# Kernel optimization log

Hardware: AMD Instinct MI355X
Metric: run time of the kernel (lower is better)

The kernel has to match this reference:

```python
import jax, jax.numpy as jnp
import numpy as np

V, E, H, K, B, T = 50000, 128, 256, 9, 128, 512
HD = H // 2  # hidden per direction


def setup_inputs() -> dict:
    key = jax.random.key(0)
    ks = jax.random.split(key, 16)
    s = 0.1
    inp = {
        "x": jax.random.randint(ks[0], (B, T), 0, V),
        "emb": jax.random.normal(ks[1], (V, E), jnp.float32) * 0.02,
        "w_ih_f": jax.random.normal(ks[2], (4 * HD, E), jnp.float32) * s,
        "w_hh_f": jax.random.normal(ks[3], (4 * HD, HD), jnp.float32) * s,
        "b_ih_f": jax.random.normal(ks[4], (4 * HD,), jnp.float32) * s,
        "b_hh_f": jax.random.normal(ks[5], (4 * HD,), jnp.float32) * s,
        "w_ih_b": jax.random.normal(ks[6], (4 * HD, E), jnp.float32) * s,
        "w_hh_b": jax.random.normal(ks[7], (4 * HD, HD), jnp.float32) * s,
        "b_ih_b": jax.random.normal(ks[8], (4 * HD,), jnp.float32) * s,
        "b_hh_b": jax.random.normal(ks[9], (4 * HD,), jnp.float32) * s,
        "W_tag": jax.random.normal(ks[10], (K, H), jnp.float32) * s,
        "b_tag": jax.random.normal(ks[11], (K,), jnp.float32) * s,
        "start_trans": jax.random.normal(ks[12], (K,), jnp.float32) * s,
        "end_trans": jax.random.normal(ks[13], (K,), jnp.float32) * s,
        "trans": jax.random.normal(ks[14], (K, K), jnp.float32) * s,
    }
    return inp


def _lstm_dir(xs, w_ih, w_hh, b_ih, b_hh, reverse):
    # xs: [T, B, E]; PyTorch gate order: i, f, g, o
    Bsz = xs.shape[1]
    hd = w_hh.shape[1]
    b = b_ih + b_hh

    def step(carry, x_t):
        h, c = carry
        gates = x_t @ w_ih.T + h @ w_hh.T + b  # [B, 4*hd]
        i, f, g, o = jnp.split(gates, 4, axis=-1)
        i = jax.nn.sigmoid(i)
        f = jax.nn.sigmoid(f)
        g = jnp.tanh(g)
        o = jax.nn.sigmoid(o)
        c = f * c + i * g
        h = o * jnp.tanh(c)
        return (h, c), h

    init = (jnp.zeros((Bsz, hd), xs.dtype), jnp.zeros((Bsz, hd), xs.dtype))
    _, hs = jax.lax.scan(step, init, xs, reverse=reverse)
    return hs  # [T, B, hd], time-ordered


def _viterbi(emissions, start_trans, end_trans, trans):
    # emissions: [T, B, K]; returns best tag path [B, T] (torchcrf decode, no mask)
    score0 = start_trans[None, :] + emissions[0]  # [B, K]

    def step(score, emis_t):
        # score[b, i] + trans[i, j] -> best over i
        cand = score[:, :, None] + trans[None, :, :]  # [B, K, K]
        bp = jnp.argmax(cand, axis=1)                 # [B, K] best prev tag
        best = jnp.max(cand, axis=1)
        return best + emis_t, bp

    final_score, bps = jax.lax.scan(step, score0, emissions[1:])  # bps: [T-1, B, K]
    final_score = final_score + end_trans[None, :]
    last_tag = jnp.argmax(final_score, axis=-1)  # [B]

    def back(tag, bp):
        prev = jnp.take_along_axis(bp, tag[:, None], axis=1)[:, 0]
        return prev, prev

    _, path = jax.lax.scan(back, last_tag, bps, reverse=True)  # [T-1, B]
    tags = jnp.concatenate([path, last_tag[None, :]], axis=0)  # [T, B]
    return tags.T.astype(jnp.int32)  # [B, T]


def reference(x, emb, w_ih_f, w_hh_f, b_ih_f, b_hh_f,
              w_ih_b, w_hh_b, b_ih_b, b_hh_b,
              W_tag, b_tag, start_trans, end_trans, trans):
    xt = x.T                        # [T, B]
    e = emb[xt]                     # [T, B, E] embedding gather
    h_f = _lstm_dir(e, w_ih_f, w_hh_f, b_ih_f, b_hh_f, reverse=False)
    h_b = _lstm_dir(e, w_ih_b, w_hh_b, b_ih_b, b_hh_b, reverse=True)
    h = jnp.concatenate([h_f, h_b], axis=-1)  # [T, B, H]
    # dropout is identity at inference
    emissions = h @ W_tag.T + b_tag           # [T, B, K]
    return _viterbi(emissions, start_trans, end_trans, trans)
```

## Files before the change

kernel.cpp:

```cpp
#include <hip/hip_runtime.h>
#include <math.h>

#define TT 512
#define BB 128
#define KK 9

__device__ __forceinline__ float fast_sigmoid(float x) {
    const float LOG2E = 1.4426950408889634f;
    float e = __builtin_amdgcn_exp2f(-x * LOG2E);
    return __builtin_amdgcn_rcpf(1.0f + e);
}
__device__ __forceinline__ float fast_tanh(float x) {
    const float LOG2E = 1.4426950408889634f;
    float a = fabsf(x);
    float e = __builtin_amdgcn_exp2f(-2.0f * a * LOG2E);
    float t = (1.0f - e) * __builtin_amdgcn_rcpf(1.0f + e);
    return copysignf(t, x);
}

__global__ __launch_bounds__(256, 3) void input_gemm(
    const int* __restrict__ x, const float* __restrict__ emb,
    const float* __restrict__ w_ih_f, const float* __restrict__ w_ih_b,
    const float* __restrict__ b_ih_f, const float* __restrict__ b_hh_f,
    const float* __restrict__ b_ih_b, const float* __restrict__ b_hh_b,
    float* __restrict__ buf_f, float* __restrict__ buf_b,
    int t0f, int t0b)
{
    const int dir = blockIdx.z;
    const int s   = blockIdx.x;
    const int n0  = blockIdx.y * 128;
    const int t   = (dir ? t0b : t0f) + s;
    const float* w  = dir ? w_ih_b : w_ih_f;
    const float* bi = dir ? b_ih_b : b_ih_f;
    const float* bh = dir ? b_hh_b : b_hh_f;
    float* dst = dir ? buf_b : buf_f;

    __shared__ __align__(16) float As[32][132];
    __shared__ __align__(16) float Bs[32][132];

    const int tid  = threadIdx.x;
    const int lrow = tid >> 3;
    const int k4   = (tid & 7) * 4;

    int tokr[4];
    #pragma unroll
    for (int p = 0; p < 4; p++) tokr[p] = x[(p * 32 + lrow) * TT + t];

    const int tx = tid & 15;
    const int ty = tid >> 4;

    float acc[8][8];
    #pragma unroll
    for (int i = 0; i < 8; i++)
        #pragma unroll
        for (int j = 0; j < 8; j++) acc[i][j] = 0.0f;

    float4 aS[4], bS[4];
    #pragma unroll
    for (int p = 0; p < 4; p++) {
        aS[p] = *(const float4*)(emb + (size_t)tokr[p] * 128 + k4);
        bS[p] = *(const float4*)(w + (size_t)(n0 + p * 32 + lrow) * 128 + k4);
    }

    for (int kc = 0; kc < 128; kc += 32) {
        __syncthreads();
        #pragma unroll
        for (int p = 0; p < 4; p++) {
            const int row = p * 32 + lrow;
            As[k4 + 0][row] = aS[p].x; As[k4 + 1][row] = aS[p].y;
            As[k4 + 2][row] = aS[p].z; As[k4 + 3][row] = aS[p].w;
            Bs[k4 + 0][row] = bS[p].x; Bs[k4 + 1][row] = bS[p].y;
            Bs[k4 + 2][row] = bS[p].z; Bs[k4 + 3][row] = bS[p].w;
        }
        __syncthreads();
        if (kc + 32 < 128) {
            #pragma unroll
            for (int p = 0; p < 4; p++) {
                aS[p] = *(const float4*)(emb + (size_t)tokr[p] * 128 + kc + 32 + k4);
                bS[p] = *(const float4*)(w + (size_t)(n0 + p * 32 + lrow) * 128 + kc + 32 + k4);
            }
        }
        #pragma unroll 8
        for (int k = 0; k < 32; k++) {
            float4 af0 = *(const float4*)&As[k][ty * 8];
            float4 af1 = *(const float4*)&As[k][ty * 8 + 4];
            float4 bf0 = *(const float4*)&Bs[k][tx * 4];
            float4 bf1 = *(const float4*)&Bs[k][64 + tx * 4];
            float a_[8] = {af0.x, af0.y, af0.z, af0.w, af1.x, af1.y, af1.z, af1.w};
            float b_[8] = {bf0.x, bf0.y, bf0.z, bf0.w, bf1.x, bf1.y, bf1.z, bf1.w};
            #pragma unroll
            for (int i = 0; i < 8; i++)
                #pragma unroll
                for (int j = 0; j < 8; j++)
                    acc[i][j] += a_[i] * b_[j];
        }
    }

    const int nb0 = n0 + tx * 4;
    const int nb1 = n0 + 64 + tx * 4;
    float bias[8];
    #pragma unroll
    for (int j = 0; j < 4; j++) {
        bias[j]     = bi[nb0 + j] + bh[nb0 + j];
        bias[4 + j] = bi[nb1 + j] + bh[nb1 + j];
    }
    #pragma unroll
    for (int i = 0; i < 8; i++) {
        int brow = ty * 8 + i;
        float* o = dst + ((size_t)s * 128 + brow) * 512;
        float4 v0, v1;
        v0.x = acc[i][0] + bias[0]; v0.y = acc[i][1] + bias[1];
        v0.z = acc[i][2] + bias[2]; v0.w = acc[i][3] + bias[3];
        v1.x = acc[i][4] + bias[4]; v1.y = acc[i][5] + bias[5];
        v1.z = acc[i][6] + bias[6]; v1.w = acc[i][7] + bias[7];
        *(float4*)(o + nb0) = v0;
        *(float4*)(o + nb1) = v1;
    }
}

__global__ __launch_bounds__(512, 2) void lstm_fused(
    const float* __restrict__ buf_f, const float* __restrict__ buf_b,
    const float* __restrict__ w_hh_f, const float* __restrict__ w_hh_b,
    float* __restrict__ h_all,
    float* __restrict__ h_state, float* __restrict__ c_state,
    const float* __restrict__ W_tag, const float* __restrict__ b_tag,
    const float* __restrict__ start_trans, const float* __restrict__ end_trans,
    const float* __restrict__ trans,
    float* __restrict__ emB, unsigned* __restrict__ flags,
    int* __restrict__ out,
    int t0f, int t0b, int C, int init, int tail)
{
    const int dir = blockIdx.x >> 7;
    const int b   = blockIdx.x & 127;
    const int j   = threadIdx.x;
    const int w_  = j >> 6;
    const int l   = j & 63;
    const int m   = l >> 2;
    const int q   = l & 3;
    const int k   = w_ * 16 + m;
    const int r   = q * 128 + k;

    unsigned snap = 0u;
    if (tail && dir == 0 && j == 0)
        snap = __hip_atomic_load(&flags[b], __ATOMIC_RELAXED, __HIP_MEMORY_SCOPE_AGENT);

    const float* whh = dir ? w_hh_b : w_hh_f;
    float wR[128];
    #pragma unroll
    for (int qq = 0; qq < 32; qq++) {
        float4 v = *(const float4*)(whh + (size_t)r * 128 + qq * 4);
        wR[4*qq+0] = v.x; wR[4*qq+1] = v.y; wR[4*qq+2] = v.z; wR[4*qq+3] = v.w;
    }

    __shared__ __align__(16) float h_lds[2][128];
    __shared__ __align__(16) float wt_s[KK * 132];
    __shared__ __align__(16) float em_s[TT * KK];
    __shared__ __align__(16) float h_tile[64 * 132];
    __shared__ unsigned char bp[TT][KK];
    __shared__ int bj_s;

    float c;
    if (init) {
        c = 0.0f;
        if (q == 0) h_lds[0][k] = 0.0f;
    } else {
        c = c_state[((size_t)dir * 128 + b) * 128 + k];
        if (q == 0) h_lds[0][k] = h_state[((size_t)dir * 128 + b) * 128 + k];
    }
    __syncthreads();

    const float* buf = dir ? buf_b : buf_f;
    const int t0     = dir ? t0b : t0f;
    const int  tl0   = dir ? (C - 1) : 0;
    const long lstep = dir ? -(long)(128 * 512) : (long)(128 * 512);

    const float* xp = buf + ((size_t)tl0 * 128 + b) * 512 + r;
    float xw = *xp;
    float h_reg = 0.0f;

    float* hdst = h_all + (size_t)(dir * BB + b) * TT * 128;

    for (int s = 0; s < C; s++) {
        const int t = t0 + (dir ? (C - 1 - s) : s);
        const int p = s & 1;
        const float* hprev = h_lds[p];

        float a0 = 0.f, a1 = 0.f, a2 = 0.f, a3 = 0.f;
        #pragma unroll
        for (int qq = 0; qq < 32; qq++) {
            float4 h4 = *(const float4*)&hprev[4 * qq];
            a0 += wR[4*qq+0] * h4.x;
            a1 += wR[4*qq+1] * h4.y;
            a2 += wR[4*qq+2] * h4.z;
            a3 += wR[4*qq+3] * h4.w;
        }
        float pre = xw + ((a0 + a1) + (a2 + a3));

        float act = (q == 2) ? fast_tanh(pre) : fast_sigmoid(pre);

        float f_ = __shfl_xor(act, 1);
        float g_ = __shfl_xor(act, 2);
        float o_ = __shfl_xor(act, 3);

        c = f_ * c + act * g_;
        h_reg = o_ * fast_tanh(c);
        if (q == 0) h_lds[p ^ 1][k] = h_reg;

        __syncthreads();

        if (s + 1 < C) { xp += lstep; xw = *xp; }
        if (q == 0)
            hdst[(size_t)t * 128 + k] = h_reg;
    }

    if (q == 0) {
        h_state[((size_t)dir * 128 + b) * 128 + k] = h_reg;
        c_state[((size_t)dir * 128 + b) * 128 + k] = c;
    }

    if (!tail) return;

    for (int f = j; f < KK * 128; f += 512)
        wt_s[(f >> 7) * 132 + (f & 127)] = W_tag[(f >> 7) * 256 + dir * 128 + (f & 127)];

    float* emdst = emB + (size_t)b * TT * KK;

    for (int tile = 0; tile < TT / 64; tile++) {
        const int tb = tile * 64;
        __syncthreads();
        #pragma unroll
        for (int it = 0; it < 4; it++) {
            const int f4 = it * 512 + j;
            const int tr = f4 >> 5;
            const int c4 = (f4 & 31) * 4;
            float4 v = *(const float4*)(hdst + (size_t)(tb + tr) * 128 + c4);
            *(float4*)&h_tile[tr * 132 + c4] = v;
        }
        __syncthreads();
        for (int task = j; task < 64 * KK; task += 512) {
            const int tl = task / 9;
            const int kk = task - tl * 9;
            const float* hp = &h_tile[tl * 132];
            const float* wp = &wt_s[kk * 132];
            float acc = 0.0f;
            #pragma unroll
            for (int i4 = 0; i4 < 32; i4++) {
                float4 h4 = *(const float4*)(hp + i4 * 4);
                float4 w4 = *(const float4*)(wp + i4 * 4);
                acc += h4.x * w4.x + h4.y * w4.y + h4.z * w4.z + h4.w * w4.w;
            }
            if (dir == 1) emdst[(size_t)tb * KK + task] = acc;
            else          em_s[tb * KK + task] = acc;
        }
    }
    __syncthreads();

    if (dir == 1) {
        if (j == 0) {
            __threadfence();
            __hip_atomic_fetch_add(&flags[b], 1u, __ATOMIC_RELEASE,
                                   __HIP_MEMORY_SCOPE_AGENT);
        }
        return;
    }

    if (j == 0) {
        while (__hip_atomic_load(&flags[b], __ATOMIC_ACQUIRE,
                                 __HIP_MEMORY_SCOPE_AGENT) == snap)
            __builtin_amdgcn_s_sleep(1);
    }
    __syncthreads();
    for (int f = j; f < TT * KK; f += 512)
        em_s[f] += emdst[f] + b_tag[f % KK];
    __syncthreads();

    if (j < 64) {
        const int lane = j;

        float trans_col[KK];
        float score = -1e30f;
        if (lane < KK) {
            #pragma unroll
            for (int i = 0; i < KK; i++) trans_col[i] = trans[i * KK + lane];
            score = start_trans[lane] + em_s[lane];
        }

        float em_cur = (lane < KK) ? em_s[KK + lane] : 0.0f;
        for (int t = 1; t < TT; t++) {
            float em_next = (t + 1 < TT && lane < KK) ? em_s[(t + 1) * KK + lane] : 0.0f;

            float my = (lane < KK) ? score : -1e30f;
            float cand[KK];
            #pragma unroll
            for (int i = 0; i < KK; i++) cand[i] = __shfl(my, i) + trans_col[i];

            float v01, v23, v45, v67, v03, v47, v07, vb_;
            int   i01, i23, i45, i67, i03, i47, i07, ib_;
            {
                bool gt;
                gt = cand[1] > cand[0]; v01 = gt ? cand[1] : cand[0]; i01 = gt ? 1 : 0;
                gt = cand[3] > cand[2]; v23 = gt ? cand[3] : cand[2]; i23 = gt ? 3 : 2;
                gt = cand[5] > cand[4]; v45 = gt ? cand[5] : cand[4]; i45 = gt ? 5 : 4;
                gt = cand[7] > cand[6]; v67 = gt ? cand[7] : cand[6]; i67 = gt ? 7 : 6;
                gt = v23 > v01; v03 = gt ? v23 : v01; i03 = gt ? i23 : i01;
                gt = v67 > v45; v47 = gt ? v67 : v45; i47 = gt ? i67 : i45;
                gt = v47 > v03; v07 = gt ? v47 : v03; i07 = gt ? i47 : i03;
                gt = cand[8] > v07; vb_ = gt ? cand[8] : v07; ib_ = gt ? 8 : i07;
            }

            if (lane < KK) {
                bp[t][lane] = (unsigned char)ib_;
                score = vb_ + em_cur;
            }
            em_cur = em_next;
        }

        float fin = (lane < KK) ? (score + end_trans[lane]) : -1e30f;
        float farr[KK];
        #pragma unroll
        for (int jx = 0; jx < KK; jx++) farr[jx] = __shfl(fin, jx);
        float v01, v23, v45, v67, v03, v47, v07, vb_;
        int   i01, i23, i45, i67, i03, i47, i07, bj;
        {
            bool gt;
            gt = farr[1] > farr[0]; v01 = gt ? farr[1] : farr[0]; i01 = gt ? 1 : 0;
            gt = farr[3] > farr[2]; v23 = gt ? farr[3] : farr[2]; i23 = gt ? 3 : 2;
            gt = farr[5] > farr[4]; v45 = gt ? farr[5] : farr[4]; i45 = gt ? 5 : 4;
            gt = farr[7] > farr[6]; v67 = gt ? farr[7] : farr[6]; i67 = gt ? 7 : 6;
            gt = v23 > v01; v03 = gt ? v23 : v01; i03 = gt ? i23 : i01;
            gt = v67 > v45; v47 = gt ? v67 : v45; i47 = gt ? i67 : i45;
            gt = v47 > v03; v07 = gt ? v47 : v03; i07 = gt ? i47 : i03;
            gt = farr[8] > v07; vb_ = gt ? farr[8] : v07; bj = gt ? 8 : i07;
        }

        if (lane == 0) {
            bj_s = bj;
            out[b * TT + (TT - 1)] = bj;
        }
    }
    __syncthreads();

    {
        unsigned char* mA = (unsigned char*)h_tile;
        unsigned char* mB = mA + TT * KK;
        #pragma unroll
        for (int i = 0; i < KK; i++)
            mA[j * KK + i] = (j >= 1) ? bp[j][i] : (unsigned char)0;
        __syncthreads();
        for (int kk = 1; kk < TT; kk <<= 1) {
            if (j >= 1) {
                if (j + kk < TT) {
                    #pragma unroll
                    for (int i = 0; i < KK; i++)
                        mB[j * KK + i] = mA[j * KK + mA[(j + kk) * KK + i]];
                } else {
                    #pragma unroll
                    for (int i = 0; i < KK; i++)
                        mB[j * KK + i] = mA[j * KK + i];
                }
            }
            __syncthreads();
            unsigned char* tmp = mA; mA = mB; mB = tmp;
        }
        if (j >= 1)
            out[b * TT + (j - 1)] = mA[j * KK + bj_s];
    }
}

extern "C" void kernel_launch(void* const* d_in, const int* in_sizes, int n_in,
                              void* d_out, int out_size, void* d_ws, size_t ws_size,
                              hipStream_t stream)
{
    const int*   x       = (const int*)  d_in[0];
    const float* emb     = (const float*)d_in[1];
    const float* w_ih_f  = (const float*)d_in[2];
    const float* w_hh_f  = (const float*)d_in[3];
    const float* b_ih_f  = (const float*)d_in[4];
    const float* b_hh_f  = (const float*)d_in[5];
    const float* w_ih_b  = (const float*)d_in[6];
    const float* w_hh_b  = (const float*)d_in[7];
    const float* b_ih_b  = (const float*)d_in[8];
    const float* b_hh_b  = (const float*)d_in[9];
    const float* W_tag   = (const float*)d_in[10];
    const float* b_tag   = (const float*)d_in[11];
    const float* start_t = (const float*)d_in[12];
    const float* end_t   = (const float*)d_in[13];
    const float* trans   = (const float*)d_in[14];
    int* out = (int*)d_out;

    const size_t em_elems    = (size_t)BB * TT * KK;
    const size_t state_elems = (size_t)2 * 128 * 128;
    const size_t hall_elems  = (size_t)2 * BB * TT * 128;

    int C = 32;
    const int cands[5] = {512, 256, 128, 64, 32};
    for (int ci = 0; ci < 5; ci++) {
        size_t need = ((size_t)2 * cands[ci] * BB * 512
                       + em_elems + 2 * state_elems + hall_elems) * sizeof(float)
                      + 1024;
        if (ws_size >= need) { C = cands[ci]; break; }
    }

    float* buf_f   = (float*)d_ws;
    float* buf_b   = buf_f + (size_t)C * BB * 512;
    float* emB     = buf_b + (size_t)C * BB * 512;
    float* h_state = emB + em_elems;
    float* c_state = h_state + state_elems;
    float* h_all   = c_state + state_elems;
    unsigned* flags = (unsigned*)(h_all + hall_elems);

    const int rounds = TT / C;
    for (int r = 0; r < rounds; r++) {
        const int t0f = r * C;
        const int t0b = TT - (r + 1) * C;
        dim3 gg(C, 4, 2);
        input_gemm<<<gg, dim3(256), 0, stream>>>(
            x, emb, w_ih_f, w_ih_b, b_ih_f, b_hh_f, b_ih_b, b_hh_b,
            buf_f, buf_b, t0f, t0b);
        lstm_fused<<<dim3(256), dim3(512), 0, stream>>>(
            buf_f, buf_b, w_hh_f, w_hh_b, h_all,
            h_state, c_state,
            W_tag, b_tag, start_t, end_t, trans,
            emB, flags, out,
            t0f, t0b, C, (r == 0) ? 1 : 0, (r == rounds - 1) ? 1 : 0);
    }
}
```

Measured before the change: 877.5 us.

## Fuse input projection GEMM into per-sequence LSTM kernel prologue

Removes the separate input_gemm launch. Each LSTM block now computes the input projection for its own sequence and time chunk in a prologue, reusing the LDS arrays as GEMM staging, and writes the result to a per-block buffer laid out [dir][b][t][gate]. The goal is to drop a kernel launch per round and make the recurrent loop's reads of precomputed gates contiguous per block. In exchange the projection now runs on only 256 blocks, serialized before the recurrence instead of spread across a wide grid, and the minimum chunk size rises to 128.

```diff
diff --git a/kernel.cpp b/kernel.cpp
--- a/kernel.cpp
+++ b/kernel.cpp
@@ -18,108 +18,12 @@
     return copysignf(t, x);
 }
 
-__global__ __launch_bounds__(256, 3) void input_gemm(
+__global__ __launch_bounds__(512, 2) void lstm_fused(
     const int* __restrict__ x, const float* __restrict__ emb,
     const float* __restrict__ w_ih_f, const float* __restrict__ w_ih_b,
     const float* __restrict__ b_ih_f, const float* __restrict__ b_hh_f,
     const float* __restrict__ b_ih_b, const float* __restrict__ b_hh_b,
-    float* __restrict__ buf_f, float* __restrict__ buf_b,
-    int t0f, int t0b)
-{
-    const int dir = blockIdx.z;
-    const int s   = blockIdx.x;
-    const int n0  = blockIdx.y * 128;
-    const int t   = (dir ? t0b : t0f) + s;
-    const float* w  = dir ? w_ih_b : w_ih_f;
-    const float* bi = dir ? b_ih_b : b_ih_f;
-    const float* bh = dir ? b_hh_b : b_hh_f;
-    float* dst = dir ? buf_b : buf_f;
-
-    __shared__ __align__(16) float As[32][132];
-    __shared__ __align__(16) float Bs[32][132];
-
-    const int tid  = threadIdx.x;
-    const int lrow = tid >> 3;
-    const int k4   = (tid & 7) * 4;
-
-    int tokr[4];
-    #pragma unroll
-    for (int p = 0; p < 4; p++) tokr[p] = x[(p * 32 + lrow) * TT + t];
-
-    const int tx = tid & 15;
-    const int ty = tid >> 4;
-
-    float acc[8][8];
-    #pragma unroll
-    for (int i = 0; i < 8; i++)
-        #pragma unroll
-        for (int j = 0; j < 8; j++) acc[i][j] = 0.0f;
-
-    float4 aS[4], bS[4];
-    #pragma unroll
-    for (int p = 0; p < 4; p++) {
-        aS[p] = *(const float4*)(emb + (size_t)tokr[p] * 128 + k4);
-        bS[p] = *(const float4*)(w + (size_t)(n0 + p * 32 + lrow) * 128 + k4);
-    }
-
-    for (int kc = 0; kc < 128; kc += 32) {
-        __syncthreads();
-        #pragma unroll
-        for (int p = 0; p < 4; p++) {
-            const int row = p * 32 + lrow;
-            As[k4 + 0][row] = aS[p].x; As[k4 + 1][row] = aS[p].y;
-            As[k4 + 2][row] = aS[p].z; As[k4 + 3][row] = aS[p].w;
-            Bs[k4 + 0][row] = bS[p].x; Bs[k4 + 1][row] = bS[p].y;
-            Bs[k4 + 2][row] = bS[p].z; Bs[k4 + 3][row] = bS[p].w;
-        }
-        __syncthreads();
-        if (kc + 32 < 128) {
-            #pragma unroll
-            for (int p = 0; p < 4; p++) {
-                aS[p] = *(const float4*)(emb + (size_t)tokr[p] * 128 + kc + 32 + k4);
-                bS[p] = *(const float4*)(w + (size_t)(n0 + p * 32 + lrow) * 128 + kc + 32 + k4);
-            }
-        }
-        #pragma unroll 8
-        for (int k = 0; k < 32; k++) {
-            float4 af0 = *(const float4*)&As[k][ty * 8];
-            float4 af1 = *(const float4*)&As[k][ty * 8 + 4];
-            float4 bf0 = *(const float4*)&Bs[k][tx * 4];
-            float4 bf1 = *(const float4*)&Bs[k][64 + tx * 4];
-            float a_[8] = {af0.x, af0.y, af0.z, af0.w, af1.x, af1.y, af1.z, af1.w};
-            float b_[8] = {bf0.x, bf0.y, bf0.z, bf0.w, bf1.x, bf1.y, bf1.z, bf1.w};
-            #pragma unroll
-            for (int i = 0; i < 8; i++)
-                #pragma unroll
-                for (int j = 0; j < 8; j++)
-                    acc[i][j] += a_[i] * b_[j];
-        }
-    }
-
-    const int nb0 = n0 + tx * 4;
-    const int nb1 = n0 + 64 + tx * 4;
-    float bias[8];
-    #pragma unroll
-    for (int j = 0; j < 4; j++) {
-        bias[j]     = bi[nb0 + j] + bh[nb0 + j];
-        bias[4 + j] = bi[nb1 + j] + bh[nb1 + j];
-    }
-    #pragma unroll
-    for (int i = 0; i < 8; i++) {
-        int brow = ty * 8 + i;
-        float* o = dst + ((size_t)s * 128 + brow) * 512;
-        float4 v0, v1;
-        v0.x = acc[i][0] + bias[0]; v0.y = acc[i][1] + bias[1];
-        v0.z = acc[i][2] + bias[2]; v0.w = acc[i][3] + bias[3];
-        v1.x = acc[i][4] + bias[4]; v1.y = acc[i][5] + bias[5];
-        v1.z = acc[i][6] + bias[6]; v1.w = acc[i][7] + bias[7];
-        *(float4*)(o + nb0) = v0;
-        *(float4*)(o + nb1) = v1;
-    }
-}
-
-__global__ __launch_bounds__(512, 2) void lstm_fused(
-    const float* __restrict__ buf_f, const float* __restrict__ buf_b,
+    float* __restrict__ buf2,
     const float* __restrict__ w_hh_f, const float* __restrict__ w_hh_b,
     float* __restrict__ h_all,
     float* __restrict__ h_state, float* __restrict__ c_state,
@@ -133,6 +37,136 @@
     const int dir = blockIdx.x >> 7;
     const int b   = blockIdx.x & 127;
     const int j   = threadIdx.x;
+
+    __shared__ __align__(16) float h_lds[2][128];
+    __shared__ __align__(16) float wt_s[KK * 132];
+    __shared__ __align__(16) float em_s[TT * KK];
+    __shared__ __align__(16) float h_tile[64 * 132];
+    __shared__ unsigned char bp[TT][KK];
+    __shared__ int bj_s;
+
+    unsigned snap = 0u;
+    if (tail && dir == 0 && j == 0)
+        snap = __hip_atomic_load(&flags[b], __ATOMIC_RELAXED, __HIP_MEMORY_SCOPE_AGENT);
+
+    const int t0 = dir ? t0b : t0f;
+
+    {
+        int*   x_s = (int*)wt_s;
+        float* As2 = em_s;
+        float* Bs2 = h_tile;
+        const float* wih = dir ? w_ih_b : w_ih_f;
+        const float* bi  = dir ? b_ih_b : b_ih_f;
+        const float* bh  = dir ? b_hh_b : b_hh_f;
+        float* myb = buf2 + (size_t)(dir * BB + b) * C * 512;
+
+        for (int f = j; f < C; f += 512) x_s[f] = x[b * TT + t0 + f];
+        __syncthreads();
+
+        const int ty  = j >> 5;
+        const int tx  = j & 31;
+        const int Atr = j >> 2;
+        const int Aq  = (j & 3) * 8;
+        const int Bgr = j >> 1;
+        const int Bq  = (j & 1) * 16;
+
+        const int ntg = C >> 7;
+        for (int gg = 0; gg < 2; gg++) {
+            const int g0 = gg * 256 + tx * 4;
+            const int g1 = g0 + 128;
+            float bias0[4], bias1[4];
+            #pragma unroll
+            for (int u = 0; u < 4; u++) {
+                bias0[u] = bi[g0 + u] + bh[g0 + u];
+                bias1[u] = bi[g1 + u] + bh[g1 + u];
+            }
+            const float* bBase = wih + (size_t)(gg * 256 + Bgr) * 128;
+
+            for (int tg = 0; tg < ntg; tg++) {
+                float acc[8][8];
+                #pragma unroll
+                for (int i = 0; i < 8; i++)
+                    #pragma unroll
+                    for (int jj = 0; jj < 8; jj++) acc[i][jj] = 0.0f;
+
+                const int tokA = x_s[tg * 128 + Atr];
+                const float* aBase = emb + (size_t)tokA * 128;
+
+                float4 aP0 = *(const float4*)(aBase + Aq);
+                float4 aP1 = *(const float4*)(aBase + Aq + 4);
+                float4 bP0 = *(const float4*)(bBase + Bq);
+                float4 bP1 = *(const float4*)(bBase + Bq + 4);
+                float4 bP2 = *(const float4*)(bBase + Bq + 8);
+                float4 bP3 = *(const float4*)(bBase + Bq + 12);
+
+                for (int kc = 0; kc < 128; kc += 32) {
+                    __syncthreads();
+                    As2[(Aq + 0) * 132 + Atr] = aP0.x;
+                    As2[(Aq + 1) * 132 + Atr] = aP0.y;
+                    As2[(Aq + 2) * 132 + Atr] = aP0.z;
+                    As2[(Aq + 3) * 132 + Atr] = aP0.w;
+                    As2[(Aq + 4) * 132 + Atr] = aP1.x;
+                    As2[(Aq + 5) * 132 + Atr] = aP1.y;
+                    As2[(Aq + 6) * 132 + Atr] = aP1.z;
+                    As2[(Aq + 7) * 132 + Atr] = aP1.w;
+                    Bs2[(Bq + 0) * 260 + Bgr] = bP0.x;
+                    Bs2[(Bq + 1) * 260 + Bgr] = bP0.y;
+                    Bs2[(Bq + 2) * 260 + Bgr] = bP0.z;
+                    Bs2[(Bq + 3) * 260 + Bgr] = bP0.w;
+                    Bs2[(Bq + 4) * 260 + Bgr] = bP1.x;
+                    Bs2[(Bq + 5) * 260 + Bgr] = bP1.y;
+                    Bs2[(Bq + 6) * 260 + Bgr] = bP1.z;
+                    Bs2[(Bq + 7) * 260 + Bgr] = bP1.w;
+                    Bs2[(Bq + 8) * 260 + Bgr] = bP2.x;
+                    Bs2[(Bq + 9) * 260 + Bgr] = bP2.y;
+                    Bs2[(Bq + 10) * 260 + Bgr] = bP2.z;
+                    Bs2[(Bq + 11) * 260 + Bgr] = bP2.w;
+                    Bs2[(Bq + 12) * 260 + Bgr] = bP3.x;
+                    Bs2[(Bq + 13) * 260 + Bgr] = bP3.y;
+                    Bs2[(Bq + 14) * 260 + Bgr] = bP3.z;
+                    Bs2[(Bq + 15) * 260 + Bgr] = bP3.w;
+                    __syncthreads();
+                    if (kc + 32 < 128) {
+                        aP0 = *(const float4*)(aBase + kc + 32 + Aq);
+                        aP1 = *(const float4*)(aBase + kc + 32 + Aq + 4);
+                        bP0 = *(const float4*)(bBase + kc + 32 + Bq);
+                        bP1 = *(const float4*)(bBase + kc + 32 + Bq + 4);
+                        bP2 = *(const float4*)(bBase + kc + 32 + Bq + 8);
+                        bP3 = *(const float4*)(bBase + kc + 32 + Bq + 12);
+                    }
+                    #pragma unroll 8
+                    for (int k = 0; k < 32; k++) {
+                        float4 af0 = *(const float4*)&As2[k * 132 + ty * 8];
+                        float4 af1 = *(const float4*)&As2[k * 132 + ty * 8 + 4];
+                        float4 bf0 = *(const float4*)&Bs2[k * 260 + tx * 4];
+                        float4 bf1 = *(const float4*)&Bs2[k * 260 + 128 + tx * 4];
+                        float a_[8] = {af0.x, af0.y, af0.z, af0.w,
+                                       af1.x, af1.y, af1.z, af1.w};
+                        float b_[8] = {bf0.x, bf0.y, bf0.z, bf0.w,
+                                       bf1.x, bf1.y, bf1.z, bf1.w};
+                        #pragma unroll
+                        for (int i = 0; i < 8; i++)
+                            #pragma unroll
+                            for (int jj = 0; jj < 8; jj++)
+                                acc[i][jj] += a_[i] * b_[jj];
+                    }
+                }
+                #pragma unroll
+                for (int i = 0; i < 8; i++) {
+                    const int tl = tg * 128 + ty * 8 + i;
+                    float* o = myb + (size_t)tl * 512;
+                    float4 v0, v1;
+                    v0.x = acc[i][0] + bias0[0]; v0.y = acc[i][1] + bias0[1];
+                    v0.z = acc[i][2] + bias0[2]; v0.w = acc[i][3] + bias0[3];
+                    v1.x = acc[i][4] + bias1[0]; v1.y = acc[i][5] + bias1[1];
+                    v1.z = acc[i][6] + bias1[2]; v1.w = acc[i][7] + bias1[3];
+                    *(float4*)(o + g0) = v0;
+                    *(float4*)(o + g1) = v1;
+                }
+            }
+        }
+    }
+
     const int w_  = j >> 6;
     const int l   = j & 63;
     const int m   = l >> 2;
@@ -140,10 +174,6 @@
     const int k   = w_ * 16 + m;
     const int r   = q * 128 + k;
 
-    unsigned snap = 0u;
-    if (tail && dir == 0 && j == 0)
-        snap = __hip_atomic_load(&flags[b], __ATOMIC_RELAXED, __HIP_MEMORY_SCOPE_AGENT);
-
     const float* whh = dir ? w_hh_b : w_hh_f;
     float wR[128];
     #pragma unroll
@@ -151,13 +181,6 @@
         float4 v = *(const float4*)(whh + (size_t)r * 128 + qq * 4);
         wR[4*qq+0] = v.x; wR[4*qq+1] = v.y; wR[4*qq+2] = v.z; wR[4*qq+3] = v.w;
     }
-
-    __shared__ __align__(16) float h_lds[2][128];
-    __shared__ __align__(16) float wt_s[KK * 132];
-    __shared__ __align__(16) float em_s[TT * KK];
-    __shared__ __align__(16) float h_tile[64 * 132];
-    __shared__ unsigned char bp[TT][KK];
-    __shared__ int bj_s;
 
     float c;
     if (init) {
@@ -169,12 +192,10 @@
     }
     __syncthreads();
 
-    const float* buf = dir ? buf_b : buf_f;
-    const int t0     = dir ? t0b : t0f;
     const int  tl0   = dir ? (C - 1) : 0;
-    const long lstep = dir ? -(long)(128 * 512) : (long)(128 * 512);
-
-    const float* xp = buf + ((size_t)tl0 * 128 + b) * 512 + r;
+    const long lstep = dir ? -(long)512 : (long)512;
+
+    const float* xp = buf2 + ((size_t)(dir * BB + b) * C + tl0) * 512 + r;
     float xw = *xp;
     float h_reg = 0.0f;
 
@@ -392,18 +413,17 @@
     const size_t state_elems = (size_t)2 * 128 * 128;
     const size_t hall_elems  = (size_t)2 * BB * TT * 128;
 
-    int C = 32;
-    const int cands[5] = {512, 256, 128, 64, 32};
-    for (int ci = 0; ci < 5; ci++) {
+    int C = 128;
+    const int cands[3] = {512, 256, 128};
+    for (int ci = 0; ci < 3; ci++) {
         size_t need = ((size_t)2 * cands[ci] * BB * 512
                        + em_elems + 2 * state_elems + hall_elems) * sizeof(float)
                       + 1024;
         if (ws_size >= need) { C = cands[ci]; break; }
     }
 
-    float* buf_f   = (float*)d_ws;
-    float* buf_b   = buf_f + (size_t)C * BB * 512;
-    float* emB     = buf_b + (size_t)C * BB * 512;
+    float* buf2    = (float*)d_ws;
+    float* emB     = buf2 + (size_t)2 * C * BB * 512;
     float* h_state = emB + em_elems;
     float* c_state = h_state + state_elems;
     float* h_all   = c_state + state_elems;
@@ -413,12 +433,9 @@
     for (int r = 0; r < rounds; r++) {
         const int t0f = r * C;
         const int t0b = TT - (r + 1) * C;
-        dim3 gg(C, 4, 2);
-        input_gemm<<<gg, dim3(256), 0, stream>>>(
+        lstm_fused<<<dim3(256), dim3(512), 0, stream>>>(
             x, emb, w_ih_f, w_ih_b, b_ih_f, b_hh_f, b_ih_b, b_hh_b,
-            buf_f, buf_b, t0f, t0b);
-        lstm_fused<<<dim3(256), dim3(512), 0, stream>>>(
-            buf_f, buf_b, w_hh_f, w_hh_b, h_all,
+            buf2, w_hh_f, w_hh_b, h_all,
             h_state, c_state,
             W_tag, b_tag, start_t, end_t, trans,
             emB, flags, out,
```

Result: faster. 850.4 us (-3.1%).
